# Kernel tuning notes

Measured on AMD Instinct MI355X. Metric: run time of the kernel, lower is better.

Reference implementation:

```python
import jax, jax.numpy as jnp
import numpy as np
from jax import lax

# 4D convolution (valid padding, stride 1) via XLA's rank-general conv.
# dimension_numbers: N=batch, C=channels, then 4 spatial axes H,W,D,T.
DN = ('NCHWDT', 'OIHWDT', 'NCHWDT')

def conv4d(x, w, b):
    y = lax.conv_general_dilated(x, w, window_strides=(1, 1, 1, 1),
                                 padding='VALID', dimension_numbers=DN)
    return y + b.reshape(1, -1, 1, 1, 1, 1)


def setup_inputs() -> dict:
    key = jax.random.key(0)
    ks = jax.random.split(key, 7)
    B = 128
    x = jax.random.normal(ks[0], (B, 1, 18, 18, 18, 18), dtype=jnp.float32)
    # conv4d(1, 5, 7): weight [out=5, in=1, 7,7,7,7]
    w1 = jax.random.normal(ks[1], (5, 1, 7, 7, 7, 7), dtype=jnp.float32) * 0.02
    b1 = jax.random.normal(ks[2], (5,), dtype=jnp.float32) * 0.02
    # conv4d(5, 10, 7): weight [10, 5, 7,7,7,7]
    w2 = jax.random.normal(ks[3], (10, 5, 7, 7, 7, 7), dtype=jnp.float32) * 0.02
    b2 = jax.random.normal(ks[4], (10,), dtype=jnp.float32) * 0.02
    # Linear(10 * 6**4, 1)
    feat = 10 * 6 ** 4  # 12960
    w_lin = jax.random.normal(ks[5], (1, feat), dtype=jnp.float32) * 0.02
    b_lin = jax.random.normal(ks[6], (1,), dtype=jnp.float32) * 0.02
    return {"x": x, "w1": w1, "b1": b1, "w2": w2, "b2": b2,
            "w_lin": w_lin, "b_lin": b_lin}


def reference(x, w1, b1, w2, b2, w_lin, b_lin):
    # head: conv4d -> ReLU -> conv4d -> ReLU
    h = jax.nn.relu(conv4d(x, w1, b1))          # [B, 5, 12,12,12,12]
    h = jax.nn.relu(conv4d(h, w2, b2))          # [B, 10, 6,6,6,6]
    # out: Flatten -> Dropout(eval: identity) -> Linear -> Sigmoid
    h = h.reshape(h.shape[0], -1)               # [B, 12960]
    logits = h @ w_lin.T + b_lin                 # [B, 1]
    return jax.nn.sigmoid(logits)
```

## Files before the change

kernel.cpp:

```cpp
#include <hip/hip_runtime.h>
#include <math.h>

typedef unsigned u32;
typedef _Float16 f16x8 __attribute__((ext_vector_type(8)));
typedef float    f32x16 __attribute__((ext_vector_type(16)));

static __device__ __forceinline__ u32 pack2(_Float16 a, _Float16 b) {
    union { _Float16 h[2]; u32 u; } v;
    v.h[0] = a; v.h[1] = b;
    return v.u;
}


__global__ __launch_bounds__(256) void pack_A1p(
    const float* __restrict__ w1, _Float16* __restrict__ A1)
{
    int i = blockIdx.x * 256 + threadIdx.x;
    if (i >= 9600) return;
    u32 outv = 0u;
    int kh = i / 1164, r = i % 1164;
    if (kh < 7 && r < 1148) {
        int kw = r / 164, r2 = r % 164;
        if (r2 < 140) {
            int kd = r2 / 20, r3 = r2 % 20;
            int oc = r3 / 4, j2 = r3 % 4;
            int j0 = 2 * j2, j1 = 2 * j2 + 1;
            const float* wb = w1 + oc * 2401 + kh * 343 + kw * 49 + kd * 7;
            _Float16 v0 = (j0 < 7) ? (_Float16)wb[j0] : (_Float16)0.f;
            _Float16 v1 = (j1 < 7) ? (_Float16)wb[j1] : (_Float16)0.f;
            outv = pack2(v0, v1);
        }
    }
    ((u32*)A1)[i] = outv;
}

__global__ __launch_bounds__(256) void pack_A2v2(
    const float* __restrict__ w2, _Float16* __restrict__ A2)
{
    int i = blockIdx.x * 256 + threadIdx.x;
    int j = i & 7;
    int lane = (i >> 3) & 63;
    int t = i >> 9;
    int k2 = t % 25; t /= 25;
    int she = t % 9;
    int ci = t / 9;
    int g = lane >> 5, m = lane & 31;
    int tap = 2 * k2 + g;
    float v = 0.f;
    if (m < 30 && tap < 49 && j < 7) {
        int dh = m / 10, oc = m % 10;
        int kh = she - dh;
        if (kh >= 0 && kh < 7) {
            int kw = tap / 7, kd = tap % 7;
            v = w2[oc * 12005 + ci * 2401 + kh * 343 + kw * 49 + kd * 7 + j];
        }
    }
    A2[i] = (_Float16)v;
}

#define C1_SLAB 9360
#define C1_AOFF 9360
#define C1_LDS  (9360 + 9600)
__global__ __launch_bounds__(256, 2) void conv1_mfma(
    const float* __restrict__ x, const _Float16* __restrict__ A1,
    const float* __restrict__ b1, _Float16* __restrict__ h1)
{
    __shared__ u32 lds[C1_LDS];
    int tid = threadIdx.x;
    int lane = tid & 63;
    int wave = tid >> 6;
    int col = lane & 31;
    int g = lane >> 5;

    int bid = (int)blockIdx.x;
    int lbid = (bid & 7) * 192 + (bid >> 3);
    int OWp = lbid % 3;
    int OH = (lbid / 3) & 3;
    int b = lbid / 12;

    int qn[3], u_[3], od_[3], ot_[3];
    #pragma unroll
    for (int s = 0; s < 3; ++s) {
        int nt = wave + 4 * s;
        int n = (nt <= 8) ? nt * 32 + col : col;
        int u = n / 144, r2 = n % 144;
        int od = r2 / 12, ot = r2 % 12;
        u_[s] = u; od_[s] = od; ot_[s] = ot;
        qn[s] = (u * 36 + od) * 52 + ot * 4;
    }

    f32x16 acc0, acc1, acc2;
    #pragma unroll
    for (int q = 0; q < 16; ++q) { acc0[q] = 0.f; acc1[q] = 0.f; acc2[q] = 0.f; }

    const float* xbase = x + (size_t)b * 104976;
    int w10 = tid / 18, id18 = tid % 18;
    int iw = 4 * OWp + w10;
    bool stager = (tid < 180);

    int mc = (col < 30) ? col : 29;
    int am_dw = mc / 15, am_dh = (mc % 15) / 5, am_oc = mc % 5;
    int jadd = 4 * (col - mc);
    int vlane = 4 * am_oc - 164 * am_dw + jadd;
    int zbase = C1_AOFF + 8312 + vlane;
    bool eLo = (am_dw == 1);
    bool e3  = (am_dw == 1) && (g == 0);
    bool e24 = (am_dw == 0) && (g == 1);
    bool eHi = (am_dw == 0);

    float2 xr[9];
    {
        const uint4* asrc = (const uint4*)A1;
        uint4* adst = (uint4*)(lds + C1_AOFF);
        #pragma unroll
        for (int i = 0; i < 10; ++i) {
            int q = tid + 256 * i;
            if (q < 2400) adst[q] = asrc[q];
        }
        if (stager) {
            const float2* src = (const float2*)(xbase + (3 * OH) * 5832 + iw * 324 + id18 * 18);
            #pragma unroll
            for (int q = 0; q < 9; ++q) xr[q] = src[q];
        }
    }

    for (int se = 0; se < 9; ++se) {
        int kh = se - am_dh;
        int vbase = (kh >= 0 && kh < 7) ? (C1_AOFF + kh * 1164 + vlane) : zbase;

        __syncthreads();
        if (stager) {
            _Float16 h[19];
            #pragma unroll
            for (int q = 0; q < 9; ++q) { h[2*q] = (_Float16)xr[q].x; h[2*q+1] = (_Float16)xr[q].y; }
            h[18] = (_Float16)0.f;
            u32 e[9], o[9];
            #pragma unroll
            for (int q = 0; q < 9; ++q) e[q] = pack2(h[2*q], h[2*q+1]);
            #pragma unroll
            for (int q = 0; q < 9; ++q) o[q] = pack2(h[2*q+1], (q < 8) ? h[2*q+2] : h[18]);
            int base = tid * 52;
            #pragma unroll
            for (int ot = 0; ot < 12; ++ot) {
                uint4 w;
                if ((ot & 1) == 0) { const int q = ot >> 1;   w = (uint4){e[q], e[q+1], e[q+2], e[q+3]}; }
                else               { const int q = (ot-1)>>1; w = (uint4){o[q], o[q+1], o[q+2], o[q+3]}; }
                *(uint4*)(&lds[base + ot * 4]) = w;
            }
        }
        __syncthreads();

        if (se < 8 && stager) {
            const float2* src = (const float2*)(xbase + (3 * OH + se + 1) * 5832 + iw * 324 + id18 * 18);
            #pragma unroll
            for (int q = 0; q < 9; ++q) xr[q] = src[q];
        }

        #pragma unroll
        for (int k2 = 0; k2 < 28; ++k2) {
            const int t0 = 2 * k2, t1 = 2 * k2 + 1;
            const int c0 = ((t0 / 7) * 18 + (t0 % 7)) * 52;
            const int c1 = ((t1 / 7) * 18 + (t1 % 7)) * 52;
            const int ca0 = 164 * (t0 / 7) + 20 * (t0 % 7);
            const int ca1 = 164 * (t1 / 7) + 20 * (t1 % 7);
            int qoff = g ? c1 : c0;
            int ca   = g ? ca1 : ca0;
            int abase;
            if (k2 <= 2)       abase = eLo ? zbase : vbase;
            else if (k2 == 3)  abase = e3  ? zbase : vbase;
            else if (k2 == 24) abase = e24 ? zbase : vbase;
            else if (k2 >= 25) abase = eHi ? zbase : vbase;
            else               abase = vbase;
            f16x8 af = *(const f16x8*)(lds + abase + ca);
            f16x8 bf0 = *(const f16x8*)(lds + qn[0] + qoff);
            f16x8 bf1 = *(const f16x8*)(lds + qn[1] + qoff);
            acc0 = __builtin_amdgcn_mfma_f32_32x32x16_f16(af, bf0, acc0, 0, 0, 0);
            acc1 = __builtin_amdgcn_mfma_f32_32x32x16_f16(af, bf1, acc1, 0, 0, 0);
            if (wave == 0) {
                f16x8 bf2 = *(const f16x8*)(lds + qn[2] + qoff);
                acc2 = __builtin_amdgcn_mfma_f32_32x32x16_f16(af, bf2, acc2, 0, 0, 0);
            }
        }
    }

    #pragma unroll
    for (int s = 0; s < 3; ++s) {
        if (s == 2 && wave != 0) continue;
        f32x16 a = (s == 0) ? acc0 : ((s == 1) ? acc1 : acc2);
        int ow_b = 4 * OWp + 2 * u_[s];
        #pragma unroll
        for (int r = 0; r < 16; ++r) {
            const int m0 = (r & 3) + 8 * (r >> 2);
            const int m1 = m0 + 4;
            const int dw0 = m0 / 15, dh0 = (m0 % 15) / 5, oc0 = m0 % 5;
            const int dw1 = m1 / 15, dh1 = (m1 % 15) / 5, oc1 = m1 % 5;
            if (m1 >= 30 && g) continue;
            int dw = g ? dw1 : dw0;
            int dh = g ? dh1 : dh0;
            int oc = g ? oc1 : oc0;
            float bv = g ? b1[oc1] : b1[oc0];
            float v = fmaxf(a[r] + bv, 0.f);
            h1[(size_t)b * 103680 + oc * 20736 + (3 * OH + dh) * 1728
               + (ow_b + dw) * 144 + od_[s] * 12 + ot_[s]] = (_Float16)v;
        }
    }
}

#define C2_SLAB 4032
#define C2_ALDS 6400
__global__ __launch_bounds__(256, 3) void conv2_mfma(
    const _Float16* __restrict__ h1, const _Float16* __restrict__ A2,
    _Float16* __restrict__ part)
{
    __shared__ u32 lds[C2_SLAB + C2_ALDS];
    int tid = threadIdx.x;
    int lane = tid & 63;
    int wave = tid >> 6;
    int col = lane & 31;
    int g = lane >> 5;

    int bid = (int)blockIdx.x;
    int lbid = (bid & 7) * 160 + (bid >> 3);
    int ci = lbid % 5;
    int OH2 = (lbid / 5) & 1;
    int b = lbid / 10;

    int qn[2], n_[2];
    #pragma unroll
    for (int s = 0; s < 2; ++s) {
        int nt = wave + 4 * s;
        int n = nt * 32 + col;
        n_[s] = n;
        int nc = (n < 216) ? n : 215;
        int ow = nc / 36, rem = nc % 36;
        int od = rem / 6, ot = rem % 6;
        qn[s] = (ow * 12 + od) * 28 + ot * 4;
    }

    f32x16 acc0, acc1;
    #pragma unroll
    for (int q = 0; q < 16; ++q) { acc0[q] = 0.f; acc1[q] = 0.f; }

    const _Float16* hbase = h1 + (size_t)b * 103680 + ci * 20736;
    const uint4* a2u = (const uint4*)(A2 + ((size_t)ci * 9) * 12800);
    int iw = tid / 12, id12 = tid % 12;
    bool stager = (tid < 144);

    uint2 xr[3]; uint4 apf[7];
    {
        if (stager) {
            const uint2* src = (const uint2*)(hbase + (3 * OH2) * 1728 + iw * 144 + id12 * 12);
            #pragma unroll
            for (int q = 0; q < 3; ++q) xr[q] = src[q];
        }
        #pragma unroll
        for (int i = 0; i < 7; ++i) { int q = tid + 256 * i; if (q < 1600) apf[i] = a2u[q]; }
    }

    for (int she = 0; she < 9; ++she) {
        __syncthreads();
        if (stager) {
            _Float16 h[14];
            *(uint2*)&h[0] = xr[0]; *(uint2*)&h[4] = xr[1]; *(uint2*)&h[8] = xr[2];
            h[12] = (_Float16)0.f;
            u32 e[6], o[6];
            #pragma unroll
            for (int q = 0; q < 6; ++q) e[q] = pack2(h[2*q], h[2*q+1]);
            #pragma unroll
            for (int q = 0; q < 6; ++q) o[q] = pack2(h[2*q+1], (q < 5) ? h[2*q+2] : h[12]);
            int base = tid * 28;
            #pragma unroll
            for (int ot = 0; ot < 6; ++ot) {
                uint4 w;
                if ((ot & 1) == 0) { const int q = ot >> 1;   w = (uint4){e[q], e[q+1], e[q+2], e[q+3]}; }
                else               { const int q = (ot-1)>>1; w = (uint4){o[q], o[q+1], o[q+2], o[q+3]}; }
                *(uint4*)(&lds[base + ot * 4]) = w;
            }
        }
        {
            uint4* adst = (uint4*)(&lds[C2_SLAB]);
            #pragma unroll
            for (int i = 0; i < 7; ++i) { int q = tid + 256 * i; if (q < 1600) adst[q] = apf[i]; }
        }
        __syncthreads();

        if (she < 8) {
            if (stager) {
                const uint2* src = (const uint2*)(hbase + (3 * OH2 + she + 1) * 1728 + iw * 144 + id12 * 12);
                #pragma unroll
                for (int q = 0; q < 3; ++q) xr[q] = src[q];
            }
            const uint4* asrc = a2u + (size_t)(she + 1) * 1600;
            #pragma unroll
            for (int i = 0; i < 7; ++i) { int q = tid + 256 * i; if (q < 1600) apf[i] = asrc[q]; }
        }

        const u32* alds = &lds[C2_SLAB];
        #pragma unroll
        for (int k2 = 0; k2 < 25; ++k2) {
            const int t0 = 2 * k2, t1 = 2 * k2 + 1;
            const int c0 = ((t0 / 7) * 12 + (t0 % 7)) * 28;
            const int c1 = (t1 < 49) ? ((t1 / 7) * 12 + (t1 % 7)) * 28 : 0;
            int qoff = g ? c1 : c0;
            f16x8 af = *(const f16x8*)(alds + (k2 * 64 + lane) * 4);
            f16x8 bf0 = *(const f16x8*)(lds + qn[0] + qoff);
            acc0 = __builtin_amdgcn_mfma_f32_32x32x16_f16(af, bf0, acc0, 0, 0, 0);
            if (wave < 3) {
                f16x8 bf1 = *(const f16x8*)(lds + qn[1] + qoff);
                acc1 = __builtin_amdgcn_mfma_f32_32x32x16_f16(af, bf1, acc1, 0, 0, 0);
            }
        }
    }

    #pragma unroll
    for (int s = 0; s < 2; ++s) {
        if (s == 1 && wave >= 3) continue;
        if (n_[s] >= 216) continue;
        f32x16 a = (s == 0) ? acc0 : acc1;
        #pragma unroll
        for (int r = 0; r < 16; ++r) {
            const int m0 = (r & 3) + 8 * (r >> 2);
            const int m1 = m0 + 4;
            const int dh0 = m0 / 10, oc0 = m0 % 10;
            const int dh1 = m1 / 10, oc1 = m1 % 10;
            if (m1 >= 30 && g) continue;
            int dh = g ? dh1 : dh0;
            int oc = g ? oc1 : oc0;
            int oh = 3 * OH2 + dh;
            part[((size_t)(ci * 768 + b * 6 + oh) * 10 + oc) * 216 + n_[s]] = (_Float16)a[r];
        }
    }
}

__global__ __launch_bounds__(256) void conv2_reduce(
    const _Float16* __restrict__ part, const float* __restrict__ b2,
    _Float16* __restrict__ h2)
{
    int flat = blockIdx.x * 256 + threadIdx.x;
    int n_loc = flat % 216;
    int t = flat / 216;
    int oc = t % 10;  t /= 10;
    int oh = t % 6;
    int b  = t / 6;
    float s = 0.f;
    #pragma unroll
    for (int ci = 0; ci < 5; ++ci)
        s += (float)part[((size_t)(ci * 768 + b * 6 + oh) * 10 + oc) * 216 + n_loc];
    s = fmaxf(s + b2[oc], 0.f);
    h2[(size_t)b * 12960 + oc * 1296 + oh * 216 + n_loc] = (_Float16)s;
}

__global__ __launch_bounds__(256) void linear_kernel(
    const _Float16* __restrict__ h2, const float* __restrict__ wl,
    const float* __restrict__ bl, float* __restrict__ out)
{
    int b = blockIdx.x;
    const _Float16* hb = h2 + (size_t)b * 12960;
    float s = 0.f;
    for (int i = threadIdx.x; i < 12960; i += 256)
        s += (float)hb[i] * wl[i];
    #pragma unroll
    for (int off = 32; off > 0; off >>= 1)
        s += __shfl_down(s, off, 64);
    __shared__ float wsum[4];
    int wave = threadIdx.x >> 6;
    if ((threadIdx.x & 63) == 0) wsum[wave] = s;
    __syncthreads();
    if (threadIdx.x == 0) {
        float tot = wsum[0] + wsum[1] + wsum[2] + wsum[3] + bl[0];
        out[b] = 1.f / (1.f + expf(-tot));
    }
}

extern "C" void kernel_launch(void* const* d_in, const int* in_sizes, int n_in,
                              void* d_out, int out_size, void* d_ws, size_t ws_size,
                              hipStream_t stream) {
    const float* x  = (const float*)d_in[0];
    const float* w1 = (const float*)d_in[1];
    const float* b1 = (const float*)d_in[2];
    const float* w2 = (const float*)d_in[3];
    const float* b2 = (const float*)d_in[4];
    const float* wl = (const float*)d_in[5];
    const float* bl = (const float*)d_in[6];
    float* out = (float*)d_out;

    _Float16* h1   = (_Float16*)d_ws;
    _Float16* A1   = h1 + 13271040;
    _Float16* A2   = A1 + 129024;
    _Float16* part = A2 + 576000;
    _Float16* h2   = part + 8294400;

    pack_A1p<<<38, 256, 0, stream>>>(w1, A1);
    pack_A2v2<<<2250, 256, 0, stream>>>(w2, A2);
    conv1_mfma<<<1536, 256, 0, stream>>>(x, A1, b1, h1);
    conv2_mfma<<<1280, 256, 0, stream>>>(h1, A2, part);
    conv2_reduce<<<6480, 256, 0, stream>>>(part, b2, h2);
    linear_kernel<<<128, 256, 0, stream>>>(h2, wl, bl, out);
}
```

Measured before the change: 287.0 us.

## Load compact per-channel conv2 weights into LDS once instead of streaming per slab

The conv2 weight pack moves from a pre-expanded layout with one tile per output-height slab (9 copies with zero-padded kh shifts) to a compact per-input-channel layout. Each block now loads all weights for its channel into LDS once and indexes by kh and tap, with a zero region for invalid rows. This removes the per-iteration global weight prefetch, the LDS rewrite and the register staging, and the packing kernel shrinks a lot. In exchange LDS use per block roughly doubles, so the launch bound drops from 3 to 2 blocks per CU, which lowers occupancy.

```diff
diff --git a/kernel.cpp b/kernel.cpp
--- a/kernel.cpp
+++ b/kernel.cpp
@@ -16,7 +16,7 @@
     const float* __restrict__ w1, _Float16* __restrict__ A1)
 {
     int i = blockIdx.x * 256 + threadIdx.x;
-    if (i >= 9600) return;
+    if (i >= 9728) return;
     u32 outv = 0u;
     int kh = i / 1164, r = i % 1164;
     if (kh < 7 && r < 1148) {
@@ -34,33 +34,30 @@
     ((u32*)A1)[i] = outv;
 }
 
-__global__ __launch_bounds__(256) void pack_A2v2(
+__global__ __launch_bounds__(256) void pack_A2p(
     const float* __restrict__ w2, _Float16* __restrict__ A2)
 {
     int i = blockIdx.x * 256 + threadIdx.x;
-    int j = i & 7;
-    int lane = (i >> 3) & 63;
-    int t = i >> 9;
-    int k2 = t % 25; t /= 25;
-    int she = t % 9;
-    int ci = t / 9;
-    int g = lane >> 5, m = lane & 31;
-    int tap = 2 * k2 + g;
-    float v = 0.f;
-    if (m < 30 && tap < 49 && j < 7) {
-        int dh = m / 10, oc = m % 10;
-        int kh = she - dh;
-        if (kh >= 0 && kh < 7) {
-            int kw = tap / 7, kd = tap % 7;
-            v = w2[oc * 12005 + ci * 2401 + kh * 343 + kw * 49 + kd * 7 + j];
-        }
-    }
-    A2[i] = (_Float16)v;
+    if (i >= 79040) return;
+    int ci = i / 15808, r = i % 15808;
+    int kh = r / 1976, r2 = r % 1976;
+    u32 outv = 0u;
+    if (kh < 7 && r2 < 1960) {
+        int kw = r2 / 280, r3 = r2 % 280;
+        int kd = r3 / 40, r4 = r3 % 40;
+        int oc = r4 / 4, j2 = r4 % 4;
+        int j0 = 2 * j2, j1 = 2 * j2 + 1;
+        const float* wb = w2 + oc * 12005 + ci * 2401 + kh * 343 + kw * 49 + kd * 7;
+        _Float16 v0 = (j0 < 7) ? (_Float16)wb[j0] : (_Float16)0.f;
+        _Float16 v1 = (j1 < 7) ? (_Float16)wb[j1] : (_Float16)0.f;
+        outv = pack2(v0, v1);
+    }
+    ((u32*)A2)[i] = outv;
 }
 
 #define C1_SLAB 9360
 #define C1_AOFF 9360
-#define C1_LDS  (9360 + 9600)
+#define C1_LDS  (9360 + 9728)
 __global__ __launch_bounds__(256, 2) void conv1_mfma(
     const float* __restrict__ x, const _Float16* __restrict__ A1,
     const float* __restrict__ b1, _Float16* __restrict__ h1)
@@ -115,7 +112,7 @@
         #pragma unroll
         for (int i = 0; i < 10; ++i) {
             int q = tid + 256 * i;
-            if (q < 2400) adst[q] = asrc[q];
+            if (q < 2432) adst[q] = asrc[q];
         }
         if (stager) {
             const float2* src = (const float2*)(xbase + (3 * OH) * 5832 + iw * 324 + id18 * 18);
@@ -207,12 +204,13 @@
 }
 
 #define C2_SLAB 4032
-#define C2_ALDS 6400
-__global__ __launch_bounds__(256, 3) void conv2_mfma(
+#define C2_AOFF 4032
+#define C2_LDS  (4032 + 15808)
+__global__ __launch_bounds__(256, 2) void conv2_mfma(
     const _Float16* __restrict__ h1, const _Float16* __restrict__ A2,
     _Float16* __restrict__ part)
 {
-    __shared__ u32 lds[C2_SLAB + C2_ALDS];
+    __shared__ u32 lds[C2_LDS];
     int tid = threadIdx.x;
     int lane = tid & 63;
     int wave = tid >> 6;
@@ -242,22 +240,35 @@
     for (int q = 0; q < 16; ++q) { acc0[q] = 0.f; acc1[q] = 0.f; }
 
     const _Float16* hbase = h1 + (size_t)b * 103680 + ci * 20736;
-    const uint4* a2u = (const uint4*)(A2 + ((size_t)ci * 9) * 12800);
     int iw = tid / 12, id12 = tid % 12;
     bool stager = (tid < 144);
 
-    uint2 xr[3]; uint4 apf[7];
+    int mc = (col < 30) ? col : 29;
+    int am_dh = mc / 10, am_oc = mc % 10;
+    int jadd = 4 * (col - mc);
+    int vlane = 4 * am_oc + jadd;
+    int zb = C2_AOFF + 13832 + vlane;
+
+    uint2 xr[3];
     {
+        const uint4* asrc = (const uint4*)A2 + (size_t)ci * 3952;
+        uint4* adst = (uint4*)(lds + C2_AOFF);
+        #pragma unroll
+        for (int i = 0; i < 16; ++i) {
+            int q = tid + 256 * i;
+            if (q < 3952) adst[q] = asrc[q];
+        }
         if (stager) {
             const uint2* src = (const uint2*)(hbase + (3 * OH2) * 1728 + iw * 144 + id12 * 12);
             #pragma unroll
             for (int q = 0; q < 3; ++q) xr[q] = src[q];
         }
-        #pragma unroll
-        for (int i = 0; i < 7; ++i) { int q = tid + 256 * i; if (q < 1600) apf[i] = a2u[q]; }
     }
 
     for (int she = 0; she < 9; ++she) {
+        int kh = she - am_dh;
+        int vb = (kh >= 0 && kh < 7) ? (C2_AOFF + kh * 1976 + vlane) : zb;
+
         __syncthreads();
         if (stager) {
             _Float16 h[14];
@@ -277,32 +288,25 @@
                 *(uint4*)(&lds[base + ot * 4]) = w;
             }
         }
-        {
-            uint4* adst = (uint4*)(&lds[C2_SLAB]);
-            #pragma unroll
-            for (int i = 0; i < 7; ++i) { int q = tid + 256 * i; if (q < 1600) adst[q] = apf[i]; }
-        }
         __syncthreads();
 
-        if (she < 8) {
-            if (stager) {
-                const uint2* src = (const uint2*)(hbase + (3 * OH2 + she + 1) * 1728 + iw * 144 + id12 * 12);
-                #pragma unroll
-                for (int q = 0; q < 3; ++q) xr[q] = src[q];
-            }
-            const uint4* asrc = a2u + (size_t)(she + 1) * 1600;
-            #pragma unroll
-            for (int i = 0; i < 7; ++i) { int q = tid + 256 * i; if (q < 1600) apf[i] = asrc[q]; }
-        }
-
-        const u32* alds = &lds[C2_SLAB];
+        if (she < 8 && stager) {
+            const uint2* src = (const uint2*)(hbase + (3 * OH2 + she + 1) * 1728 + iw * 144 + id12 * 12);
+            #pragma unroll
+            for (int q = 0; q < 3; ++q) xr[q] = src[q];
+        }
+
         #pragma unroll
         for (int k2 = 0; k2 < 25; ++k2) {
             const int t0 = 2 * k2, t1 = 2 * k2 + 1;
             const int c0 = ((t0 / 7) * 12 + (t0 % 7)) * 28;
             const int c1 = (t1 < 49) ? ((t1 / 7) * 12 + (t1 % 7)) * 28 : 0;
+            const int a0 = 280 * (t0 / 7) + 40 * (t0 % 7);
+            const int a1 = (t1 < 49) ? (280 * (t1 / 7) + 40 * (t1 % 7)) : 0;
             int qoff = g ? c1 : c0;
-            f16x8 af = *(const f16x8*)(alds + (k2 * 64 + lane) * 4);
+            int ca   = g ? a1 : a0;
+            int ab = (k2 == 24 && g) ? zb : vb;
+            f16x8 af = *(const f16x8*)(lds + ab + ca);
             f16x8 bf0 = *(const f16x8*)(lds + qn[0] + qoff);
             acc0 = __builtin_amdgcn_mfma_f32_32x32x16_f16(af, bf0, acc0, 0, 0, 0);
             if (wave < 3) {
@@ -391,7 +395,7 @@
     _Float16* h2   = part + 8294400;
 
     pack_A1p<<<38, 256, 0, stream>>>(w1, A1);
-    pack_A2v2<<<2250, 256, 0, stream>>>(w2, A2);
+    pack_A2p<<<309, 256, 0, stream>>>(w2, A2);
     conv1_mfma<<<1536, 256, 0, stream>>>(x, A1, b1, h1);
     conv2_mfma<<<1280, 256, 0, stream>>>(h1, A2, part);
     conv2_reduce<<<6480, 256, 0, stream>>>(part, b2, h2);
```

New measurement: 237.4 us. 17.3% less time.
